# Kernel tuning notes

Measured on AMD Instinct MI355X. Metric: run time of the kernel, lower is better.

Reference implementation:

```python
import jax, jax.numpy as jnp
import numpy as np

N_NODES = 50000
N_EDGES = 800000
N_LABEL_EDGES = 200000
IN_CH = 256
HID = 64
OUT_CH = 64


def gcn_conv(x, W, b, edge_index, n_nodes):
    """PyG GCNConv: symmetric-normalized aggregation with self-loops.
    out[col] = sum_row norm(row,col) * (x @ W)[row] + b
    """
    xw = x @ W  # [N, out]
    loops = jnp.arange(n_nodes, dtype=edge_index.dtype)
    row = jnp.concatenate([edge_index[0], loops])  # source
    col = jnp.concatenate([edge_index[1], loops])  # target
    deg = jax.ops.segment_sum(jnp.ones_like(col, dtype=xw.dtype), col, num_segments=n_nodes)
    dis = jnp.where(deg > 0, jax.lax.rsqrt(deg), 0.0)
    norm = dis[row] * dis[col]  # [E+N]
    out = jax.ops.segment_sum(xw[row] * norm[:, None], col, num_segments=n_nodes)
    return out + b


def setup_inputs() -> dict:
    key = jax.random.key(0)
    k0, k1, k2, k3, k4 = jax.random.split(key, 5)
    x = jax.random.normal(k0, (N_NODES, IN_CH), dtype=jnp.float32)
    edge_index = jax.random.randint(k1, (2, N_EDGES), 0, N_NODES, dtype=jnp.int32)
    edge_label_index = jax.random.randint(k2, (2, N_LABEL_EDGES), 0, N_NODES, dtype=jnp.int32)
    W1 = jax.random.normal(k3, (IN_CH, HID), dtype=jnp.float32) * (1.0 / np.sqrt(IN_CH))
    b1 = jnp.zeros((HID,), dtype=jnp.float32)
    W2 = jax.random.normal(k4, (HID, OUT_CH), dtype=jnp.float32) * (1.0 / np.sqrt(HID))
    b2 = jnp.zeros((OUT_CH,), dtype=jnp.float32)
    return {"x": x, "edge_index": edge_index, "edge_label_index": edge_label_index,
            "W1": W1, "b1": b1, "W2": W2, "b2": b2}


def reference(x, edge_index, edge_label_index, W1, b1, W2, b2):
    n = x.shape[0]
    # encode: two GCNConv layers with ReLU between
    h = jax.nn.relu(gcn_conv(x, W1, b1, edge_index, n))
    z = gcn_conv(h, W2, b2, edge_index, n)
    # decode: gather node pairs, elementwise multiply, sum over features
    src, dst = edge_label_index[0], edge_label_index[1]
    return jnp.sum(z[src] * z[dst], axis=1)  # [N_LABEL_EDGES]
```

## Files before the change

### kernel.cpp

```cpp
#include <hip/hip_runtime.h>
#include <hip/hip_bf16.h>


constexpr int NC = 512;
constexpr int NBPAD = 256;
constexpr int BSHIFT = 8;

using short8 = __attribute__((ext_vector_type(8))) short;
using f32x4 = __attribute__((ext_vector_type(4))) float;

__device__ __forceinline__ unsigned short f2bf(float f) {
    unsigned u = __float_as_uint(f);
    return (unsigned short)((u + 0x7FFF + ((u >> 16) & 1)) >> 16);
}
__device__ __forceinline__ float bf2f(unsigned short h) {
    return __uint_as_float(((unsigned)h) << 16);
}
__device__ __forceinline__ float4 bf4_to_f4(ushort4 u) {
    return make_float4(bf2f(u.x), bf2f(u.y), bf2f(u.z), bf2f(u.w));
}

__global__ __launch_bounds__(256) void hist_kernel(const int* __restrict__ col,
                                                   int* __restrict__ histCM,
                                                   int* __restrict__ bsums, int E, int CE) {
    __shared__ int hl[NBPAD];
    const int t = threadIdx.x, c = blockIdx.x;
    hl[t] = 0;
    __syncthreads();
    const int s = c * CE, e = min(E, s + CE);
    for (int i = s + t; i < e; i += 256) atomicAdd(&hl[col[i] >> BSHIFT], 1);
    __syncthreads();
    const int v = hl[t];
    histCM[c * NBPAD + t] = v;
    if (v) atomicAdd(&bsums[t], v);
}

__global__ __launch_bounds__(256) void rowscan_kernel(const int* __restrict__ histCM,
                                                      const int* __restrict__ bsums,
                                                      int* __restrict__ offsBM) {
    __shared__ int red[256];
    __shared__ int sc[256];
    const int t = threadIdx.x, b = blockIdx.x;
    red[t] = (t < b) ? bsums[t] : 0;
    __syncthreads();
    for (int off = 128; off > 0; off >>= 1) {
        if (t < off) red[t] += red[t + off];
        __syncthreads();
    }
    const int base = red[0];
    const int a0 = histCM[(2 * t) * NBPAD + b];
    const int a1 = histCM[(2 * t + 1) * NBPAD + b];
    const int ps = a0 + a1;
    sc[t] = ps;
    __syncthreads();
    for (int off = 1; off < 256; off <<= 1) {
        int u = (t >= off) ? sc[t - off] : 0;
        __syncthreads();
        sc[t] += u;
        __syncthreads();
    }
    const int excl = sc[t] - ps;
    offsBM[b * NC + 2 * t] = base + excl;
    offsBM[b * NC + 2 * t + 1] = base + excl + a0;
}

__global__ __launch_bounds__(256) void reorder_kernel(const int* __restrict__ row,
                                                      const int* __restrict__ col,
                                                      const int* __restrict__ offsBM,
                                                      int* __restrict__ part, int E, int CE) {
    __shared__ int cur[NBPAD];
    const int t = threadIdx.x, c = blockIdx.x;
    cur[t] = offsBM[t * NC + c];
    __syncthreads();
    const int s = c * CE, e = min(E, s + CE);
    for (int i = s + t; i < e; i += 256) {
        const int r = row[i], cl = col[i];
        const int p = atomicAdd(&cur[cl >> BSHIFT], 1);
        part[p] = (r << 8) | (cl & 255);
    }
}

__global__ __launch_bounds__(256) void bucket_csr_kernel(const int* __restrict__ part,
                                                         const int* __restrict__ offsBM,
                                                         int* __restrict__ csr,
                                                         int* __restrict__ offs,
                                                         float* __restrict__ dis,
                                                         int N, int E, int nbk) {
    __shared__ int cnt[256];
    __shared__ int sc[256];
    const int t = threadIdx.x, b = blockIdx.x;
    const int base = b << BSHIFT;
    const int bstart = offsBM[b * NC];
    const int bend = (b + 1 < NBPAD) ? offsBM[(b + 1) * NC] : E;
    const int m = bend - bstart;
    cnt[t] = 0;
    __syncthreads();
    for (int i = t; i < m; i += 256) atomicAdd(&cnt[part[bstart + i] & 255], 1);
    __syncthreads();
    const int v = cnt[t];
    sc[t] = v;
    __syncthreads();
    for (int off = 1; off < 256; off <<= 1) {
        int u = (t >= off) ? sc[t - off] : 0;
        __syncthreads();
        sc[t] += u;
        __syncthreads();
    }
    const int excl = sc[t] - v;
    const int node = base + t;
    if (node < N) {
        offs[node] = bstart + excl;
        dis[node] = rsqrtf((float)(v + 1));
    }
    sc[t] = excl;
    __syncthreads();
    for (int i = t; i < m; i += 256) {
        const int pc = part[bstart + i];
        const int p = atomicAdd(&sc[pc & 255], 1);
        csr[bstart + p] = pc >> 8;
    }
    if (b == nbk - 1 && t == 0) offs[N] = E;
}

__global__ __launch_bounds__(256) void pack_kernel(const float* __restrict__ W1,
                                                   const float* __restrict__ W2,
                                                   unsigned short* __restrict__ Wp1,
                                                   unsigned short* __restrict__ Wp2,
                                                   int* __restrict__ bsums) {
    const int k = threadIdx.x;
    if (blockIdx.x == 0) {
        bsums[k] = 0;
        for (int c = 0; c < 64; ++c)
            Wp1[((k >> 3) * 64 + c) * 8 + (k & 7)] = f2bf(W1[k * 64 + c]);
    } else if (k < 64) {
        for (int c = 0; c < 64; ++c)
            Wp2[((k >> 3) * 64 + c) * 8 + (k & 7)] = f2bf(W2[k * 64 + c]);
    }
}

template <int K>
__global__ __launch_bounds__(256) void gemm_mfma(const float* __restrict__ X,
                                                 const unsigned short* __restrict__ Wp,
                                                 const float* __restrict__ rowscale,
                                                 unsigned short* __restrict__ Y, int nrows) {
    const int tid = threadIdx.x;
    const int wv = tid >> 6;
    const int lane = tid & 63;
    const int m = lane & 15;
    const int quad = lane >> 4;
    const int rowbase = blockIdx.x * 64 + wv * 16;

    int grow = rowbase + m;
    if (grow >= nrows) grow = nrows - 1;
    const float* xrow = X + (long)grow * K + quad * 8;

    f32x4 acc0 = {0.f, 0.f, 0.f, 0.f};
    f32x4 acc1 = acc0, acc2 = acc0, acc3 = acc0;

    #pragma unroll
    for (int ks = 0; ks < K / 32; ++ks) {
        const float4 a0 = *(const float4*)(xrow + ks * 32);
        const float4 a1 = *(const float4*)(xrow + ks * 32 + 4);
        short8 af;
        af[0] = (short)f2bf(a0.x); af[1] = (short)f2bf(a0.y);
        af[2] = (short)f2bf(a0.z); af[3] = (short)f2bf(a0.w);
        af[4] = (short)f2bf(a1.x); af[5] = (short)f2bf(a1.y);
        af[6] = (short)f2bf(a1.z); af[7] = (short)f2bf(a1.w);
        const unsigned short* bp = Wp + (size_t)((ks * 4 + quad) * 64) * 8;
        const short8 b0 = *(const short8*)(bp + (0 * 16 + m) * 8);
        const short8 b1 = *(const short8*)(bp + (1 * 16 + m) * 8);
        const short8 b2 = *(const short8*)(bp + (2 * 16 + m) * 8);
        const short8 b3 = *(const short8*)(bp + (3 * 16 + m) * 8);
        acc0 = __builtin_amdgcn_mfma_f32_16x16x32_bf16(af, b0, acc0, 0, 0, 0);
        acc1 = __builtin_amdgcn_mfma_f32_16x16x32_bf16(af, b1, acc1, 0, 0, 0);
        acc2 = __builtin_amdgcn_mfma_f32_16x16x32_bf16(af, b2, acc2, 0, 0, 0);
        acc3 = __builtin_amdgcn_mfma_f32_16x16x32_bf16(af, b3, acc3, 0, 0, 0);
    }

    #pragma unroll
    for (int reg = 0; reg < 4; ++reg) {
        const int orow = rowbase + quad * 4 + reg;
        if (orow < nrows) {
            const float d = rowscale[orow];
            unsigned short* yp = Y + (size_t)orow * 64 + m;
            yp[0]  = f2bf(d * acc0[reg]);
            yp[16] = f2bf(d * acc1[reg]);
            yp[32] = f2bf(d * acc2[reg]);
            yp[48] = f2bf(d * acc3[reg]);
        }
    }
}

__device__ __forceinline__ void acc8(float* a, short8 v) {
    #pragma unroll
    for (int j = 0; j < 8; ++j) a[j] += bf2f((unsigned short)v[j]);
}

__global__ __launch_bounds__(256) void agg_gemm_fused(const unsigned short* __restrict__ xs,
                                                      const int* __restrict__ csr,
                                                      const int* __restrict__ offs,
                                                      const float* __restrict__ dis,
                                                      const float* __restrict__ b1,
                                                      const unsigned short* __restrict__ Wp2,
                                                      unsigned short* __restrict__ Y, int n) {
    const int tid = threadIdx.x;
    const int wv = tid >> 6;
    const int lane = tid & 63;
    const int m = lane & 15;
    const int q = lane >> 4;
    const int rowbase = blockIdx.x * 64 + wv * 16;

    int i = rowbase + m;
    if (i >= n) i = n - 1;
    const int off_lo = q * 8;

    float alo[8], ahi[8];
    {
        const unsigned short* xrow = xs + (size_t)i * 64;
        const short8 s0 = *(const short8*)(xrow + off_lo);
        const short8 s1 = *(const short8*)(xrow + 32 + off_lo);
        #pragma unroll
        for (int j = 0; j < 8; ++j) { alo[j] = bf2f((unsigned short)s0[j]); ahi[j] = bf2f((unsigned short)s1[j]); }
    }

    const int s = offs[i];
    const int e = offs[i + 1];
    int j = s;
    int r0 = 0, r1 = 0, r2 = 0, r3 = 0;
    if (j + 3 < e) { r0 = csr[j]; r1 = csr[j + 1]; r2 = csr[j + 2]; r3 = csr[j + 3]; }
    while (j + 3 < e) {
        const int jn = j + 4;
        const int c0 = min(jn,     e - 1), c1 = min(jn + 1, e - 1);
        const int c2 = min(jn + 2, e - 1), c3 = min(jn + 3, e - 1);
        const int n0 = csr[c0], n1 = csr[c1], n2 = csr[c2], n3 = csr[c3];
        const short8 v0l = *(const short8*)(xs + (size_t)r0 * 64 + off_lo);
        const short8 v0h = *(const short8*)(xs + (size_t)r0 * 64 + 32 + off_lo);
        const short8 v1l = *(const short8*)(xs + (size_t)r1 * 64 + off_lo);
        const short8 v1h = *(const short8*)(xs + (size_t)r1 * 64 + 32 + off_lo);
        const short8 v2l = *(const short8*)(xs + (size_t)r2 * 64 + off_lo);
        const short8 v2h = *(const short8*)(xs + (size_t)r2 * 64 + 32 + off_lo);
        const short8 v3l = *(const short8*)(xs + (size_t)r3 * 64 + off_lo);
        const short8 v3h = *(const short8*)(xs + (size_t)r3 * 64 + 32 + off_lo);
        acc8(alo, v0l); acc8(ahi, v0h);
        acc8(alo, v1l); acc8(ahi, v1h);
        acc8(alo, v2l); acc8(ahi, v2h);
        acc8(alo, v3l); acc8(ahi, v3h);
        r0 = n0; r1 = n1; r2 = n2; r3 = n3;
        j = jn;
    }
    for (; j < e; ++j) {
        const int r = csr[j];
        const short8 vl = *(const short8*)(xs + (size_t)r * 64 + off_lo);
        const short8 vh = *(const short8*)(xs + (size_t)r * 64 + 32 + off_lo);
        acc8(alo, vl); acc8(ahi, vh);
    }

    const float di = dis[i];
    float bl[8], bh[8];
    *(float4*)&bl[0] = *(const float4*)(b1 + off_lo);
    *(float4*)&bl[4] = *(const float4*)(b1 + off_lo + 4);
    *(float4*)&bh[0] = *(const float4*)(b1 + 32 + off_lo);
    *(float4*)&bh[4] = *(const float4*)(b1 + 32 + off_lo + 4);
    short8 ha, hb;
    #pragma unroll
    for (int jj = 0; jj < 8; ++jj) {
        ha[jj] = (short)f2bf(fmaxf(fmaf(alo[jj], di, bl[jj]), 0.f));
        hb[jj] = (short)f2bf(fmaxf(fmaf(ahi[jj], di, bh[jj]), 0.f));
    }

    const unsigned short* bplo = Wp2 + (size_t)(q * 64) * 8;
    const unsigned short* bphi = Wp2 + (size_t)((4 + q) * 64) * 8;
    f32x4 c0 = {0.f, 0.f, 0.f, 0.f};
    f32x4 c1 = c0, c2 = c0, c3 = c0;
    const short8 w0l = *(const short8*)(bplo + (0 * 16 + m) * 8);
    const short8 w1l = *(const short8*)(bplo + (1 * 16 + m) * 8);
    const short8 w2l = *(const short8*)(bplo + (2 * 16 + m) * 8);
    const short8 w3l = *(const short8*)(bplo + (3 * 16 + m) * 8);
    const short8 w0h = *(const short8*)(bphi + (0 * 16 + m) * 8);
    const short8 w1h = *(const short8*)(bphi + (1 * 16 + m) * 8);
    const short8 w2h = *(const short8*)(bphi + (2 * 16 + m) * 8);
    const short8 w3h = *(const short8*)(bphi + (3 * 16 + m) * 8);
    c0 = __builtin_amdgcn_mfma_f32_16x16x32_bf16(ha, w0l, c0, 0, 0, 0);
    c0 = __builtin_amdgcn_mfma_f32_16x16x32_bf16(hb, w0h, c0, 0, 0, 0);
    c1 = __builtin_amdgcn_mfma_f32_16x16x32_bf16(ha, w1l, c1, 0, 0, 0);
    c1 = __builtin_amdgcn_mfma_f32_16x16x32_bf16(hb, w1h, c1, 0, 0, 0);
    c2 = __builtin_amdgcn_mfma_f32_16x16x32_bf16(ha, w2l, c2, 0, 0, 0);
    c2 = __builtin_amdgcn_mfma_f32_16x16x32_bf16(hb, w2h, c2, 0, 0, 0);
    c3 = __builtin_amdgcn_mfma_f32_16x16x32_bf16(ha, w3l, c3, 0, 0, 0);
    c3 = __builtin_amdgcn_mfma_f32_16x16x32_bf16(hb, w3h, c3, 0, 0, 0);

    #pragma unroll
    for (int reg = 0; reg < 4; ++reg) {
        const int orow = rowbase + q * 4 + reg;
        if (orow < n) {
            const float d2 = dis[orow];
            unsigned short* yp = Y + (size_t)orow * 64 + m;
            yp[0]  = f2bf(d2 * c0[reg]);
            yp[16] = f2bf(d2 * c1[reg]);
            yp[32] = f2bf(d2 * c2[reg]);
            yp[48] = f2bf(d2 * c3[reg]);
        }
    }
}

template <bool RELU, bool OUT_BF16>
__global__ __launch_bounds__(256) void agg_kernel(const unsigned short* __restrict__ xs,
                                                  const int* __restrict__ csr,
                                                  const int* __restrict__ offs,
                                                  const float* __restrict__ dis,
                                                  const float* __restrict__ bias,
                                                  void* __restrict__ out, int n) {
    const int t = threadIdx.x;
    const int fl = t & 15;
    const int i = blockIdx.x * 16 + (t >> 4);
    if (i >= n) return;
    float4 acc = bf4_to_f4(*(const ushort4*)&xs[(long)i * 64 + fl * 4]);
    const int s = offs[i];
    const int e = offs[i + 1];
    int j = s;
    int r0 = 0, r1 = 0, r2 = 0, r3 = 0;
    if (j + 3 < e) { r0 = csr[j]; r1 = csr[j + 1]; r2 = csr[j + 2]; r3 = csr[j + 3]; }
    while (j + 3 < e) {
        const int jn = j + 4;
        const int c0 = min(jn,     e - 1), c1 = min(jn + 1, e - 1);
        const int c2 = min(jn + 2, e - 1), c3 = min(jn + 3, e - 1);
        const int n0 = csr[c0], n1 = csr[c1], n2 = csr[c2], n3 = csr[c3];
        const float4 v0 = bf4_to_f4(*(const ushort4*)&xs[(long)r0 * 64 + fl * 4]);
        const float4 v1 = bf4_to_f4(*(const ushort4*)&xs[(long)r1 * 64 + fl * 4]);
        const float4 v2 = bf4_to_f4(*(const ushort4*)&xs[(long)r2 * 64 + fl * 4]);
        const float4 v3 = bf4_to_f4(*(const ushort4*)&xs[(long)r3 * 64 + fl * 4]);
        acc.x += (v0.x + v1.x) + (v2.x + v3.x);
        acc.y += (v0.y + v1.y) + (v2.y + v3.y);
        acc.z += (v0.z + v1.z) + (v2.z + v3.z);
        acc.w += (v0.w + v1.w) + (v2.w + v3.w);
        r0 = n0; r1 = n1; r2 = n2; r3 = n3;
        j = jn;
    }
    for (; j < e; ++j) {
        const int r = csr[j];
        const float4 v = bf4_to_f4(*(const ushort4*)&xs[(long)r * 64 + fl * 4]);
        acc.x += v.x; acc.y += v.y; acc.z += v.z; acc.w += v.w;
    }
    const float di = dis[i];
    const float4 b = *(const float4*)&bias[fl * 4];
    float4 o;
    o.x = fmaf(acc.x, di, b.x); o.y = fmaf(acc.y, di, b.y);
    o.z = fmaf(acc.z, di, b.z); o.w = fmaf(acc.w, di, b.w);
    if (RELU) {
        o.x = fmaxf(o.x, 0.f); o.y = fmaxf(o.y, 0.f);
        o.z = fmaxf(o.z, 0.f); o.w = fmaxf(o.w, 0.f);
    }
    if (OUT_BF16) {
        ushort4 ov;
        ov.x = f2bf(o.x); ov.y = f2bf(o.y); ov.z = f2bf(o.z); ov.w = f2bf(o.w);
        *(ushort4*)&((unsigned short*)out)[(long)i * 64 + fl * 4] = ov;
    } else {
        *(float4*)&((float*)out)[(long)i * 64 + fl * 4] = o;
    }
}

__global__ __launch_bounds__(256) void decode_kernel(const unsigned short* __restrict__ z,
                                                     const int* __restrict__ src,
                                                     const int* __restrict__ dst,
                                                     float* __restrict__ out, int L) {
    const int t = blockIdx.x * 256 + threadIdx.x;
    const int e = t >> 4;
    const int fl = t & 15;
    if (e >= L) return;
    const int s = src[e];
    const int d = dst[e];
    const float4 a = bf4_to_f4(*(const ushort4*)&z[(long)s * 64 + fl * 4]);
    const float4 b = bf4_to_f4(*(const ushort4*)&z[(long)d * 64 + fl * 4]);
    float p = a.x * b.x + a.y * b.y + a.z * b.z + a.w * b.w;
    p += __shfl_xor(p, 8); p += __shfl_xor(p, 4);
    p += __shfl_xor(p, 2); p += __shfl_xor(p, 1);
    if (fl == 0) out[e] = p;
}

extern "C" void kernel_launch(void* const* d_in, const int* in_sizes, int n_in,
                              void* d_out, int out_size, void* d_ws, size_t ws_size,
                              hipStream_t stream) {
    const float* x   = (const float*)d_in[0];
    const int*   ei  = (const int*)d_in[1];
    const int*   eli = (const int*)d_in[2];
    const float* W1  = (const float*)d_in[3];
    const float* b1  = (const float*)d_in[4];
    const float* W2  = (const float*)d_in[5];
    const float* b2  = (const float*)d_in[6];
    float* out = (float*)d_out;

    const int N = in_sizes[0] / 256;
    const int E = in_sizes[1] / 2;
    const int L = in_sizes[2] / 2;
    const int* row = ei;
    const int* col = ei + E;
    const int* src = eli;
    const int* dst = eli + L;

    char* w = (char*)d_ws;
    unsigned short* xs1 = (unsigned short*)w;  w += (size_t)N * 64 * 2;
    unsigned short* xs2 = (unsigned short*)w;  w += (size_t)N * 64 * 2;
    unsigned short* z = (unsigned short*)w;  w += (size_t)N * 64 * 2;
    int*   csr = (int*)w;    w += (size_t)E * 4;
    int*   offs = (int*)w;   w += (size_t)(N + 1) * 4;
    float* dis = (float*)w;  w += (size_t)N * 4;
    int*   part = (int*)w;   w += (size_t)E * 4;
    int* histCM = (int*)w;   w += (size_t)NC * NBPAD * 4;
    int* offsBM = (int*)w;   w += (size_t)NBPAD * NC * 4;
    int* bsums  = (int*)w;   w += NBPAD * 4;
    unsigned short* Wp1 = (unsigned short*)w;  w += (size_t)256 * 64 * 2;
    unsigned short* Wp2 = (unsigned short*)w;  w += (size_t)64 * 64 * 2;

    const int CE = (E + NC - 1) / NC;
    const int nbk = (N + (1 << BSHIFT) - 1) >> BSHIFT;

    pack_kernel<<<2, 256, 0, stream>>>(W1, W2, Wp1, Wp2, bsums);
    hist_kernel<<<NC, 256, 0, stream>>>(col, histCM, bsums, E, CE);
    rowscan_kernel<<<NBPAD, 256, 0, stream>>>(histCM, bsums, offsBM);
    reorder_kernel<<<NC, 256, 0, stream>>>(row, col, offsBM, part, E, CE);
    bucket_csr_kernel<<<nbk, 256, 0, stream>>>(part, offsBM, csr, offs, dis, N, E, nbk);

    gemm_mfma<256><<<(N + 63) / 64, 256, 0, stream>>>(x, Wp1, dis, xs1, N);
    agg_gemm_fused<<<(N + 63) / 64, 256, 0, stream>>>(xs1, csr, offs, dis, b1, Wp2, xs2, N);
    agg_kernel<false, true><<<(N + 15) / 16, 256, 0, stream>>>(xs2, csr, offs, dis, b2, z, N);
    decode_kernel<<<(L + 15) / 16, 256, 0, stream>>>(z, src, dst, out, L);
}
```

Before: 205.4 us.

## Parallelize weight packing, transpose histogram layout, widen CSR blocks and per-row aggregation

Weight packing is spread over many blocks with one element per thread instead of two serial threads-per-row loops. The histogram is stored bucket-major so the row scan can read contiguous int2 pairs. The bucket CSR build uses 1024-thread blocks. The second-layer aggregation gives each row a quarter-wave lane group with 16-byte loads, and decode uses 8 lanes per edge with 16-byte loads. Together these aim to cut serial setup latency and improve memory access width, at the cost of more per-thread registers and idle threads in the scan phase of the CSR kernel.

```diff
diff --git a/kernel.cpp b/kernel.cpp
--- a/kernel.cpp
+++ b/kernel.cpp
@@ -20,8 +20,27 @@
     return make_float4(bf2f(u.x), bf2f(u.y), bf2f(u.z), bf2f(u.w));
 }
 
+__global__ __launch_bounds__(256) void pack_kernel(const float* __restrict__ W1,
+                                                   const float* __restrict__ W2,
+                                                   unsigned short* __restrict__ Wp1,
+                                                   unsigned short* __restrict__ Wp2,
+                                                   int* __restrict__ bsums) {
+    const int t = threadIdx.x, b = blockIdx.x;
+    if (b == 0) {
+        bsums[t] = 0;
+    } else if (b <= 64) {
+        const int idx = (b - 1) * 256 + t;
+        const int k = idx >> 6, c = idx & 63;
+        Wp1[((k >> 3) * 64 + c) * 8 + (k & 7)] = f2bf(W1[idx]);
+    } else {
+        const int idx = (b - 65) * 256 + t;
+        const int k = idx >> 6, c = idx & 63;
+        Wp2[((k >> 3) * 64 + c) * 8 + (k & 7)] = f2bf(W2[idx]);
+    }
+}
+
 __global__ __launch_bounds__(256) void hist_kernel(const int* __restrict__ col,
-                                                   int* __restrict__ histCM,
+                                                   int* __restrict__ histBM,
                                                    int* __restrict__ bsums, int E, int CE) {
     __shared__ int hl[NBPAD];
     const int t = threadIdx.x, c = blockIdx.x;
@@ -31,11 +50,11 @@
     for (int i = s + t; i < e; i += 256) atomicAdd(&hl[col[i] >> BSHIFT], 1);
     __syncthreads();
     const int v = hl[t];
-    histCM[c * NBPAD + t] = v;
+    histBM[t * NC + c] = v;
     if (v) atomicAdd(&bsums[t], v);
 }
 
-__global__ __launch_bounds__(256) void rowscan_kernel(const int* __restrict__ histCM,
+__global__ __launch_bounds__(256) void rowscan_kernel(const int* __restrict__ histBM,
                                                       const int* __restrict__ bsums,
                                                       int* __restrict__ offsBM) {
     __shared__ int red[256];
@@ -48,8 +67,8 @@
         __syncthreads();
     }
     const int base = red[0];
-    const int a0 = histCM[(2 * t) * NBPAD + b];
-    const int a1 = histCM[(2 * t + 1) * NBPAD + b];
+    const int2 a = *(const int2*)&histBM[b * NC + 2 * t];
+    const int a0 = a.x, a1 = a.y;
     const int ps = a0 + a1;
     sc[t] = ps;
     __syncthreads();
@@ -80,12 +99,12 @@
     }
 }
 
-__global__ __launch_bounds__(256) void bucket_csr_kernel(const int* __restrict__ part,
-                                                         const int* __restrict__ offsBM,
-                                                         int* __restrict__ csr,
-                                                         int* __restrict__ offs,
-                                                         float* __restrict__ dis,
-                                                         int N, int E, int nbk) {
+__global__ __launch_bounds__(1024) void bucket_csr_kernel(const int* __restrict__ part,
+                                                          const int* __restrict__ offsBM,
+                                                          int* __restrict__ csr,
+                                                          int* __restrict__ offs,
+                                                          float* __restrict__ dis,
+                                                          int N, int E, int nbk) {
     __shared__ int cnt[256];
     __shared__ int sc[256];
     const int t = threadIdx.x, b = blockIdx.x;
@@ -93,49 +112,36 @@
     const int bstart = offsBM[b * NC];
     const int bend = (b + 1 < NBPAD) ? offsBM[(b + 1) * NC] : E;
     const int m = bend - bstart;
-    cnt[t] = 0;
-    __syncthreads();
-    for (int i = t; i < m; i += 256) atomicAdd(&cnt[part[bstart + i] & 255], 1);
-    __syncthreads();
-    const int v = cnt[t];
-    sc[t] = v;
+    if (t < 256) cnt[t] = 0;
+    __syncthreads();
+    for (int i = t; i < m; i += 1024) atomicAdd(&cnt[part[bstart + i] & 255], 1);
+    __syncthreads();
+    int v = 0;
+    if (t < 256) { v = cnt[t]; sc[t] = v; }
     __syncthreads();
     for (int off = 1; off < 256; off <<= 1) {
-        int u = (t >= off) ? sc[t - off] : 0;
+        int u = 0;
+        if (t >= off && t < 256) u = sc[t - off];
         __syncthreads();
-        sc[t] += u;
+        if (t < 256) sc[t] += u;
         __syncthreads();
     }
-    const int excl = sc[t] - v;
-    const int node = base + t;
-    if (node < N) {
-        offs[node] = bstart + excl;
-        dis[node] = rsqrtf((float)(v + 1));
-    }
-    sc[t] = excl;
-    __syncthreads();
-    for (int i = t; i < m; i += 256) {
+    if (t < 256) {
+        const int excl = sc[t] - v;
+        const int node = base + t;
+        if (node < N) {
+            offs[node] = bstart + excl;
+            dis[node] = rsqrtf((float)(v + 1));
+        }
+        sc[t] = excl;
+    }
+    __syncthreads();
+    for (int i = t; i < m; i += 1024) {
         const int pc = part[bstart + i];
         const int p = atomicAdd(&sc[pc & 255], 1);
         csr[bstart + p] = pc >> 8;
     }
     if (b == nbk - 1 && t == 0) offs[N] = E;
-}
-
-__global__ __launch_bounds__(256) void pack_kernel(const float* __restrict__ W1,
-                                                   const float* __restrict__ W2,
-                                                   unsigned short* __restrict__ Wp1,
-                                                   unsigned short* __restrict__ Wp2,
-                                                   int* __restrict__ bsums) {
-    const int k = threadIdx.x;
-    if (blockIdx.x == 0) {
-        bsums[k] = 0;
-        for (int c = 0; c < 64; ++c)
-            Wp1[((k >> 3) * 64 + c) * 8 + (k & 7)] = f2bf(W1[k * 64 + c]);
-    } else if (k < 64) {
-        for (int c = 0; c < 64; ++c)
-            Wp2[((k >> 3) * 64 + c) * 8 + (k & 7)] = f2bf(W2[k * 64 + c]);
-    }
 }
 
 template <int K>
@@ -303,18 +309,32 @@
     }
 }
 
-template <bool RELU, bool OUT_BF16>
-__global__ __launch_bounds__(256) void agg_kernel(const unsigned short* __restrict__ xs,
-                                                  const int* __restrict__ csr,
-                                                  const int* __restrict__ offs,
-                                                  const float* __restrict__ dis,
-                                                  const float* __restrict__ bias,
-                                                  void* __restrict__ out, int n) {
-    const int t = threadIdx.x;
-    const int fl = t & 15;
-    const int i = blockIdx.x * 16 + (t >> 4);
-    if (i >= n) return;
-    float4 acc = bf4_to_f4(*(const ushort4*)&xs[(long)i * 64 + fl * 4]);
+__global__ __launch_bounds__(256) void agg_wave(const unsigned short* __restrict__ xs,
+                                                const int* __restrict__ csr,
+                                                const int* __restrict__ offs,
+                                                const float* __restrict__ dis,
+                                                const float* __restrict__ bias,
+                                                unsigned short* __restrict__ Y, int n) {
+    const int tid = threadIdx.x;
+    const int wv = tid >> 6;
+    const int lane = tid & 63;
+    const int m = lane & 15;
+    const int q = lane >> 4;
+    const int rowbase = blockIdx.x * 64 + wv * 16;
+
+    int i = rowbase + m;
+    if (i >= n) i = n - 1;
+    const int off_lo = q * 8;
+
+    float alo[8], ahi[8];
+    {
+        const unsigned short* xrow = xs + (size_t)i * 64;
+        const short8 s0 = *(const short8*)(xrow + off_lo);
+        const short8 s1 = *(const short8*)(xrow + 32 + off_lo);
+        #pragma unroll
+        for (int j = 0; j < 8; ++j) { alo[j] = bf2f((unsigned short)s0[j]); ahi[j] = bf2f((unsigned short)s1[j]); }
+    }
+
     const int s = offs[i];
     const int e = offs[i + 1];
     int j = s;
@@ -325,38 +345,42 @@
         const int c0 = min(jn,     e - 1), c1 = min(jn + 1, e - 1);
         const int c2 = min(jn + 2, e - 1), c3 = min(jn + 3, e - 1);
         const int n0 = csr[c0], n1 = csr[c1], n2 = csr[c2], n3 = csr[c3];
-        const float4 v0 = bf4_to_f4(*(const ushort4*)&xs[(long)r0 * 64 + fl * 4]);
-        const float4 v1 = bf4_to_f4(*(const ushort4*)&xs[(long)r1 * 64 + fl * 4]);
-        const float4 v2 = bf4_to_f4(*(const ushort4*)&xs[(long)r2 * 64 + fl * 4]);
-        const float4 v3 = bf4_to_f4(*(const ushort4*)&xs[(long)r3 * 64 + fl * 4]);
-        acc.x += (v0.x + v1.x) + (v2.x + v3.x);
-        acc.y += (v0.y + v1.y) + (v2.y + v3.y);
-        acc.z += (v0.z + v1.z) + (v2.z + v3.z);
-        acc.w += (v0.w + v1.w) + (v2.w + v3.w);
+        const short8 v0l = *(const short8*)(xs + (size_t)r0 * 64 + off_lo);
+        const short8 v0h = *(const short8*)(xs + (size_t)r0 * 64 + 32 + off_lo);
+        const short8 v1l = *(const short8*)(xs + (size_t)r1 * 64 + off_lo);
+        const short8 v1h = *(const short8*)(xs + (size_t)r1 * 64 + 32 + off_lo);
+        const short8 v2l = *(const short8*)(xs + (size_t)r2 * 64 + off_lo);
+        const short8 v2h = *(const short8*)(xs + (size_t)r2 * 64 + 32 + off_lo);
+        const short8 v3l = *(const short8*)(xs + (size_t)r3 * 64 + off_lo);
+        const short8 v3h = *(const short8*)(xs + (size_t)r3 * 64 + 32 + off_lo);
+        acc8(alo, v0l); acc8(ahi, v0h);
+        acc8(alo, v1l); acc8(ahi, v1h);
+        acc8(alo, v2l); acc8(ahi, v2h);
+        acc8(alo, v3l); acc8(ahi, v3h);
         r0 = n0; r1 = n1; r2 = n2; r3 = n3;
         j = jn;
     }
     for (; j < e; ++j) {
         const int r = csr[j];
-        const float4 v = bf4_to_f4(*(const ushort4*)&xs[(long)r * 64 + fl * 4]);
-        acc.x += v.x; acc.y += v.y; acc.z += v.z; acc.w += v.w;
-    }
+        const short8 vl = *(const short8*)(xs + (size_t)r * 64 + off_lo);
+        const short8 vh = *(const short8*)(xs + (size_t)r * 64 + 32 + off_lo);
+        acc8(alo, vl); acc8(ahi, vh);
+    }
+
     const float di = dis[i];
-    const float4 b = *(const float4*)&bias[fl * 4];
-    float4 o;
-    o.x = fmaf(acc.x, di, b.x); o.y = fmaf(acc.y, di, b.y);
-    o.z = fmaf(acc.z, di, b.z); o.w = fmaf(acc.w, di, b.w);
-    if (RELU) {
-        o.x = fmaxf(o.x, 0.f); o.y = fmaxf(o.y, 0.f);
-        o.z = fmaxf(o.z, 0.f); o.w = fmaxf(o.w, 0.f);
-    }
-    if (OUT_BF16) {
-        ushort4 ov;
-        ov.x = f2bf(o.x); ov.y = f2bf(o.y); ov.z = f2bf(o.z); ov.w = f2bf(o.w);
-        *(ushort4*)&((unsigned short*)out)[(long)i * 64 + fl * 4] = ov;
-    } else {
-        *(float4*)&((float*)out)[(long)i * 64 + fl * 4] = o;
-    }
+    float bl[8], bh[8];
+    *(float4*)&bl[0] = *(const float4*)(bias + off_lo);
+    *(float4*)&bl[4] = *(const float4*)(bias + off_lo + 4);
+    *(float4*)&bh[0] = *(const float4*)(bias + 32 + off_lo);
+    *(float4*)&bh[4] = *(const float4*)(bias + 32 + off_lo + 4);
+    short8 ol, oh;
+    #pragma unroll
+    for (int jj = 0; jj < 8; ++jj) {
+        ol[jj] = (short)f2bf(fmaf(alo[jj], di, bl[jj]));
+        oh[jj] = (short)f2bf(fmaf(ahi[jj], di, bh[jj]));
+    }
+    *(short8*)(Y + (size_t)i * 64 + off_lo) = ol;
+    *(short8*)(Y + (size_t)i * 64 + 32 + off_lo) = oh;
 }
 
 __global__ __launch_bounds__(256) void decode_kernel(const unsigned short* __restrict__ z,
@@ -364,16 +388,18 @@
                                                      const int* __restrict__ dst,
                                                      float* __restrict__ out, int L) {
     const int t = blockIdx.x * 256 + threadIdx.x;
-    const int e = t >> 4;
-    const int fl = t & 15;
+    const int e = t >> 3;
+    const int fl = t & 7;
     if (e >= L) return;
     const int s = src[e];
     const int d = dst[e];
-    const float4 a = bf4_to_f4(*(const ushort4*)&z[(long)s * 64 + fl * 4]);
-    const float4 b = bf4_to_f4(*(const ushort4*)&z[(long)d * 64 + fl * 4]);
-    float p = a.x * b.x + a.y * b.y + a.z * b.z + a.w * b.w;
-    p += __shfl_xor(p, 8); p += __shfl_xor(p, 4);
-    p += __shfl_xor(p, 2); p += __shfl_xor(p, 1);
+    const short8 a = *(const short8*)&z[(long)s * 64 + fl * 8];
+    const short8 b = *(const short8*)&z[(long)d * 64 + fl * 8];
+    float p = 0.f;
+    #pragma unroll
+    for (int j = 0; j < 8; ++j)
+        p = fmaf(bf2f((unsigned short)a[j]), bf2f((unsigned short)b[j]), p);
+    p += __shfl_xor(p, 4); p += __shfl_xor(p, 2); p += __shfl_xor(p, 1);
     if (fl == 0) out[e] = p;
 }
 
@@ -405,7 +431,7 @@
     int*   offs = (int*)w;   w += (size_t)(N + 1) * 4;
     float* dis = (float*)w;  w += (size_t)N * 4;
     int*   part = (int*)w;   w += (size_t)E * 4;
-    int* histCM = (int*)w;   w += (size_t)NC * NBPAD * 4;
+    int* histBM = (int*)w;   w += (size_t)NBPAD * NC * 4;
     int* offsBM = (int*)w;   w += (size_t)NBPAD * NC * 4;
     int* bsums  = (int*)w;   w += NBPAD * 4;
     unsigned short* Wp1 = (unsigned short*)w;  w += (size_t)256 * 64 * 2;
@@ -414,14 +440,14 @@
     const int CE = (E + NC - 1) / NC;
     const int nbk = (N + (1 << BSHIFT) - 1) >> BSHIFT;
 
-    pack_kernel<<<2, 256, 0, stream>>>(W1, W2, Wp1, Wp2, bsums);
-    hist_kernel<<<NC, 256, 0, stream>>>(col, histCM, bsums, E, CE);
-    rowscan_kernel<<<NBPAD, 256, 0, stream>>>(histCM, bsums, offsBM);
+    pack_kernel<<<81, 256, 0, stream>>>(W1, W2, Wp1, Wp2, bsums);
+    hist_kernel<<<NC, 256, 0, stream>>>(col, histBM, bsums, E, CE);
+    rowscan_kernel<<<NBPAD, 256, 0, stream>>>(histBM, bsums, offsBM);
     reorder_kernel<<<NC, 256, 0, stream>>>(row, col, offsBM, part, E, CE);
-    bucket_csr_kernel<<<nbk, 256, 0, stream>>>(part, offsBM, csr, offs, dis, N, E, nbk);
+    bucket_csr_kernel<<<nbk, 1024, 0, stream>>>(part, offsBM, csr, offs, dis, N, E, nbk);
 
     gemm_mfma<256><<<(N + 63) / 64, 256, 0, stream>>>(x, Wp1, dis, xs1, N);
     agg_gemm_fused<<<(N + 63) / 64, 256, 0, stream>>>(xs1, csr, offs, dis, b1, Wp2, xs2, N);
-    agg_kernel<false, true><<<(N + 15) / 16, 256, 0, stream>>>(xs2, csr, offs, dis, b2, z, N);
-    decode_kernel<<<(L + 15) / 16, 256, 0, stream>>>(z, src, dst, out, L);
-}
+    agg_wave<<<(N + 63) / 64, 256, 0, stream>>>(xs2, csr, offs, dis, b2, z, N);
+    decode_kernel<<<(L * 8 + 255) / 256, 256, 0, stream>>>(z, src, dst, out, L);
+}
```

Result: faster. 201.0 us (median of 2 runs) (-2.2%).
